# Kernel tuning notes

Hardware: AMD Instinct MI355X
Metric: run time of the kernel (lower is better)

## Reference

```python
import jax, jax.numpy as jnp
import numpy as np

B, T, E, H2, V, NT = 256, 192, 300, 256, 11626, 13  # batch, max_len, embed, hidden_dim, vocab, num_tags
START, STOP = 0, 10
NEG = -10000.0


def setup_inputs() -> dict:
    key = jax.random.key(0)
    ks = jax.random.split(key, 13)
    H = H2 // 2
    s = 0.1
    trans = jax.random.normal(ks[12], (NT, NT), dtype=jnp.float32)
    trans = trans.at[START, :].set(NEG).at[:, STOP].set(NEG)
    return {
        "sentence": jax.random.randint(ks[0], (B, T), 0, V),
        "seq_len": jax.random.randint(ks[1], (B,), 1, T + 1),  # lengths >= 1
        "tags": jax.random.randint(ks[2], (B, T), 0, 10),
        "embedding": jax.random.normal(ks[3], (V, E), dtype=jnp.float32) * s,
        "W_ih_f": jax.random.normal(ks[4], (4 * H, E), dtype=jnp.float32) * s,
        "W_hh_f": jax.random.normal(ks[5], (4 * H, H), dtype=jnp.float32) * s,
        "b_f": jnp.zeros((4 * H,), jnp.float32),
        "W_ih_b": jax.random.normal(ks[6], (4 * H, E), dtype=jnp.float32) * s,
        "W_hh_b": jax.random.normal(ks[7], (4 * H, H), dtype=jnp.float32) * s,
        "b_b": jnp.zeros((4 * H,), jnp.float32),
        "W_fc": jax.random.normal(ks[8], (NT, H2), dtype=jnp.float32) * s,
        "b_fc": jnp.zeros((NT,), jnp.float32),
        "transitions": trans,
    }


def _rev_within_len(x, lens):
    # reverse each sequence's first `len` positions (mimics packed-sequence reverse dir)
    t = jnp.arange(x.shape[1])
    idx = jnp.where(t[None, :] < lens[:, None], lens[:, None] - 1 - t[None, :], t[None, :])
    return jnp.take_along_axis(x, idx[:, :, None], axis=1)


def _lstm_dir(x, lens, W_ih, W_hh, b):
    # x: [B,T,E] -> [B,T,H]; PyTorch gate order i,f,g,o; padded steps frozen + zeroed output
    Bx, Tx, _ = x.shape
    H = W_hh.shape[1]
    mask = (jnp.arange(Tx)[None, :] < lens[:, None]).astype(x.dtype)  # [B,T]
    gx = jnp.einsum('bte,ge->btg', x, W_ih) + b  # precompute input projections

    def step(carry, inp):
        h, c = carry
        g_x, m = inp  # [B,4H], [B,1]
        g = g_x + h @ W_hh.T
        i, f, gg, o = jnp.split(g, 4, axis=-1)
        c_new = jax.nn.sigmoid(f) * c + jax.nn.sigmoid(i) * jnp.tanh(gg)
        h_new = jax.nn.sigmoid(o) * jnp.tanh(c_new)
        h = jnp.where(m > 0, h_new, h)
        c = jnp.where(m > 0, c_new, c)
        return (h, c), h * m

    h0 = jnp.zeros((Bx, H), x.dtype)
    _, hs = jax.lax.scan(step, (h0, h0), (gx.transpose(1, 0, 2), mask.T[:, :, None]))
    return hs.transpose(1, 0, 2)


def _crf_nll(feats, tags, transitions):
    # feats: [B,T,NT]; iterate over ALL T padded positions (faithful to source)
    def fwd_step(alpha, feat):
        # alpha_new[b,j] = logsumexp_i(alpha[b,i] + trans[j,i]) + feat[b,j]
        nxt = jax.nn.logsumexp(alpha[:, None, :] + transitions[None, :, :], axis=-1) + feat
        return nxt, None

    alpha0 = jnp.full((feats.shape[0], NT), NEG, feats.dtype).at[:, START].set(0.0)
    alphaT, _ = jax.lax.scan(fwd_step, alpha0, feats.transpose(1, 0, 2))
    fwd_score = jax.nn.logsumexp(alphaT + transitions[STOP][None, :], axis=-1)  # [B]

    tags_ext = jnp.concatenate([jnp.full((feats.shape[0], 1), START, tags.dtype), tags], axis=1)
    trans_sc = transitions[tags_ext[:, 1:], tags_ext[:, :-1]].sum(-1)
    emit_sc = jnp.take_along_axis(feats, tags[:, :, None], axis=2)[:, :, 0].sum(-1)
    gold = trans_sc + emit_sc + transitions[STOP, tags[:, -1]]
    return fwd_score - gold  # [B]


def reference(sentence, seq_len, tags, embedding, W_ih_f, W_hh_f, b_f,
              W_ih_b, W_hh_b, b_b, W_fc, b_fc, transitions):
    lens = jnp.clip(seq_len, 1, T)  # seq_len.clamp(max=192)
    emb = embedding[sentence]  # [B,T,E]
    h_f = _lstm_dir(emb, lens, W_ih_f, W_hh_f, b_f)
    h_b = _rev_within_len(_lstm_dir(_rev_within_len(emb, lens), lens, W_ih_b, W_hh_b, b_b), lens)
    out = jnp.concatenate([h_f, h_b], axis=-1)  # [B,T,H2]
    feats = jnp.einsum('bth,gh->btg', out, W_fc) + b_fc  # [B,T,NT]
    nll = _crf_nll(feats, tags, transitions)
    return nll.mean()
```

## Files before the change

kernel.cpp:

```cpp
#include <hip/hip_runtime.h>
#include <hip/hip_bf16.h>


#define B_   256
#define T_   192
#define E_   300
#define KP   320
#define H_   128
#define G4   512
#define NG   1024
#define NT_  13
#define NEGV -10000.0f
#define HSTR 144

typedef __attribute__((ext_vector_type(8))) short bf16x8;
typedef __attribute__((ext_vector_type(4))) float f32x4;
typedef __attribute__((ext_vector_type(4))) unsigned short u16x4;

__device__ __forceinline__ unsigned short f2bf(float f) {
    return (unsigned short)(__float_as_uint(f) >> 16);
}
__device__ __forceinline__ float bf2f(unsigned short h) {
    return __uint_as_float(((unsigned)h) << 16);
}
__device__ __forceinline__ float sigf(float x) {
    return __builtin_amdgcn_rcpf(1.0f + __expf(-x));
}
__device__ __forceinline__ float tanhfast(float x) {
    return __builtin_amdgcn_rcpf(1.0f + __expf(-2.0f * x)) * 2.0f - 1.0f;
}
__device__ __forceinline__ void barrier_lgkm() {
    asm volatile("s_waitcnt lgkmcnt(0)\n\ts_barrier" ::: "memory");
}

__global__ void pack_kernel(const float* __restrict__ Wf, const float* __restrict__ Wb,
                            const float* __restrict__ Whf, const float* __restrict__ Whb,
                            const float* __restrict__ emb, const int* __restrict__ sent,
                            unsigned short* __restrict__ Wp, unsigned short* __restrict__ Whp,
                            unsigned short* __restrict__ A) {
    int blk = blockIdx.x;
    int k = threadIdx.x;
    if (blk < NG) {
        float v = 0.0f;
        if (k < E_) v = (blk < G4) ? Wf[blk * E_ + k] : Wb[(blk - G4) * E_ + k];
        Wp[blk * KP + k] = f2bf(v);
    } else if (blk < NG + 1024) {
        int t = blk - NG;
        int d = t >> 9, g = t & 511;
        if (k < H_) {
            const float* src = d ? Whb : Whf;
            float v = src[g * H_ + k];
            int w = (g >> 4) & 7, j = g >> 7, colq = g & 15;
            int kc = k >> 5, quad = (k >> 3) & 3, e = k & 7;
            Whp[((((size_t)(d * 8 + w) * 4 + j) * 4 + kc) * 64 + quad * 16 + colq) * 8 + e] = f2bf(v);
        }
    } else {
        int m = blk - NG - 1024;
        int tok = sent[m];
        float v = 0.0f;
        if (k < E_) v = emb[(size_t)tok * E_ + k];
        A[(size_t)m * KP + k] = f2bf(v);
    }
}

__global__ __launch_bounds__(256, 2) void gemm_kernel(const unsigned short* __restrict__ A,
                                                      const unsigned short* __restrict__ Bw,
                                                      const float* __restrict__ bF,
                                                      const float* __restrict__ bB,
                                                      unsigned short* __restrict__ C) {
    __shared__ __align__(16) unsigned short As[128 * 64];
    __shared__ __align__(16) unsigned short Bs[128 * 64];
    const int tid  = threadIdx.x;
    const int lane = tid & 63;
    const int wave = tid >> 6;
    const int wr = wave >> 1, wc = wave & 1;
    const int colL = lane & 15;
    const int mBase = blockIdx.y * 128;
    const int bx = blockIdx.x;
    const int d  = bx >> 2;
    const int w0 = (bx & 3) * 2;
    f32x4 acc[4][4] = {};
    for (int k0 = 0; k0 < KP; k0 += 64) {
        #pragma unroll
        for (int j = 0; j < 4; j++) {
            int c   = tid + 256 * j;
            int row = c >> 3;
            int col = (c & 7) * 8;
            *(uint4*)(As + row * 64 + col) = *(const uint4*)(A + (size_t)(mBase + row) * KP + k0 + col);
            int ws = row >> 6, jj = (row >> 4) & 3, cc = row & 15;
            int srcrow = d * 512 + (8 * jj + w0 + ws) * 16 + cc;
            *(uint4*)(Bs + row * 64 + col) = *(const uint4*)(Bw + (size_t)srcrow * KP + k0 + col);
        }
        __syncthreads();
        #pragma unroll
        for (int ks = 0; ks < 2; ks++) {
            bf16x8 af[4], bfr[4];
            #pragma unroll
            for (int i = 0; i < 4; i++) {
                int arow = wr * 64 + i * 16 + colL;
                af[i]  = *(const bf16x8*)(As + arow * 64 + ks * 32 + (lane >> 4) * 8);
                int brow = wc * 64 + i * 16 + colL;
                bfr[i] = *(const bf16x8*)(Bs + brow * 64 + ks * 32 + (lane >> 4) * 8);
            }
            #pragma unroll
            for (int i = 0; i < 4; i++)
                #pragma unroll
                for (int n2 = 0; n2 < 4; n2++)
                    acc[i][n2] = __builtin_amdgcn_mfma_f32_16x16x32_bf16(af[i], bfr[n2], acc[i][n2], 0, 0, 0);
        }
        __syncthreads();
    }
    const float* bias_d = d ? bB : bF;
    float bj[4];
    #pragma unroll
    for (int n2 = 0; n2 < 4; n2++) bj[n2] = bias_d[(8 * n2 + w0 + wc) * 16 + colL];
    #pragma unroll
    for (int i = 0; i < 4; i++)
        #pragma unroll
        for (int r = 0; r < 4; r++) {
            int row = mBase + wr * 64 + i * 16 + (lane >> 4) * 4 + r;
            u16x4 v;
            #pragma unroll
            for (int n2 = 0; n2 < 4; n2++) v[n2] = f2bf(acc[i][n2][r] + bj[n2]);
            *(u16x4*)(C + (size_t)row * NG + d * 512 + (w0 + wc) * 64 + colL * 4) = v;
        }
}

__global__ __launch_bounds__(576, 1) void lstm_kernel(const unsigned short* __restrict__ gxP,
                                                      const unsigned short* __restrict__ Whp,
                                                      const int* __restrict__ seq_len,
                                                      const float* __restrict__ Wfc,
                                                      float* __restrict__ featsF,
                                                      float* __restrict__ featsB) {
    __shared__ __align__(16) unsigned short hL[2][16 * HSTR];
    __shared__ int Ls[4];
    __shared__ int maxLs;
    const int tid  = threadIdx.x;
    const int wave = tid >> 6;
    const int lane = tid & 63;
    const int col  = lane & 15;
    const int quad = lane >> 4;
    const int dir  = blockIdx.x & 1;
    const int b0   = (blockIdx.x >> 1) * 4;
    float* fOut = dir ? featsB : featsF;

    if (tid < 4) Ls[tid] = min(max(seq_len[b0 + tid], 1), T_);
    __syncthreads();
    if (tid == 0) { int m = 0; for (int i = 0; i < 4; i++) m = max(m, Ls[i]); maxLs = m; }
    __syncthreads();
    const int maxL = maxLs;
    const int Lq = Ls[quad];
    const int dNG = dir ? -NG : NG;

    bf16x8 Bf[4][4];
    bf16x8 Wf8[4];
    const unsigned short* rb = nullptr;
    int ofs2 = 0;
    u16x4 gx0v = {}, gx1v = {};
    float* fb = nullptr;
    int foff = 0;

    if (wave < 8) {
        #pragma unroll
        for (int j = 0; j < 4; j++)
            #pragma unroll
            for (int kc = 0; kc < 4; kc++)
                Bf[j][kc] = *(const bf16x8*)(Whp +
                    ((((size_t)(dir * 8 + wave) * 4 + j) * 4 + kc) * 64 + lane) * 8);
        int row = b0 + quad;
        int p0 = dir ? (Lq - 1) : 0;
        rb = gxP + ((size_t)(row * T_ + p0)) * NG + dir * 512 + wave * 64 + col * 4;
        gx0v = *(const u16x4*)(rb);
        gx1v = *(const u16x4*)(rb + ((Lq > 1) ? dNG : 0));
        ofs2 = min(2, Lq - 1) * dNG;
    } else {
        #pragma unroll
        for (int kc = 0; kc < 4; kc++)
            #pragma unroll
            for (int e = 0; e < 8; e++) {
                float v = (col < NT_) ? Wfc[col * 256 + dir * H_ + kc * 32 + quad * 8 + e] : 0.0f;
                Wf8[kc][e] = (short)f2bf(v);
            }
        fb = fOut + (size_t)(b0 + quad) * T_ * NT_ + col;
        foff = (dir ? (Lq - 1) : 0) * NT_;
    }
    const int fd = dir ? -NT_ : NT_;

    float cst = 0.0f;
    bf16x8 Af[4];
    #pragma unroll
    for (int kc = 0; kc < 4; kc++)
        #pragma unroll
        for (int e = 0; e < 8; e++) Af[kc][e] = 0;

    auto step_body = [&](int s, u16x4& gxs, int par) {
        if (wave < 8) {
            f32x4 acc[4];
            #pragma unroll
            for (int j = 0; j < 4; j++) {
                acc[j][0] = bf2f(gxs[j]);
                acc[j][1] = 0.f; acc[j][2] = 0.f; acc[j][3] = 0.f;
            }
            gxs = *(const u16x4*)(rb + ofs2);
            ofs2 = (s + 3 < Lq) ? ofs2 + dNG : ofs2;
            #pragma unroll
            for (int kc = 0; kc < 4; kc++)
                #pragma unroll
                for (int j = 0; j < 4; j++)
                    acc[j] = __builtin_amdgcn_mfma_f32_16x16x32_bf16(Af[kc], Bf[j][kc], acc[j], 0, 0, 0);
            float cn = sigf(acc[1][0]) * cst + sigf(acc[0][0]) * tanhfast(acc[2][0]);
            cst = cn;
            float hn = sigf(acc[3][0]) * tanhfast(cn);
            hL[par][(quad * 4) * HSTR + wave * 16 + col] = f2bf(hn);
        }
        barrier_lgkm();
        #pragma unroll
        for (int kc = 0; kc < 4; kc++)
            Af[kc] = *(const bf16x8*)(&hL[par][col * HSTR + kc * 32 + quad * 8]);
        if (wave == 8) {
            f32x4 fc = (f32x4){0.f, 0.f, 0.f, 0.f};
            #pragma unroll
            for (int kc = 0; kc < 4; kc++)
                fc = __builtin_amdgcn_mfma_f32_16x16x32_bf16(Af[kc], Wf8[kc], fc, 0, 0, 0);
            if (col < NT_ && s < Lq) fb[foff] = fc[0];
            foff += fd;
        }
    };

    for (int s = 0; s < maxL; s += 2) {
        step_body(s, gx0v, 0);
        if (s + 1 < maxL) step_body(s + 1, gx1v, 1);
    }
}

__global__ __launch_bounds__(64) void crf_kernel(const float* __restrict__ fF,
                                                 const float* __restrict__ fB,
                                                 const float* __restrict__ bfc,
                                                 const float* __restrict__ trans,
                                                 const int* __restrict__ tags,
                                                 const int* __restrict__ seq_len,
                                                 float* __restrict__ nll) {
    __shared__ __align__(16) float al[16];
    __shared__ __align__(16) float feat_lds[2 * 208];
    __shared__ float Tlds[NT_ * NT_];
    const int lane = threadIdx.x;
    const int b = blockIdx.x;
    const int Lb = min(max(seq_len[b], 1), T_);
    const float* fFb = fF + (size_t)b * T_ * NT_;
    const float* fBb = fB + (size_t)b * T_ * NT_;
    const int* tg = tags + (size_t)b * T_;

    for (int i = lane; i < NT_ * NT_; i += 64) Tlds[i] = trans[i];

    const int jc = min(lane, NT_ - 1);
    float Tj[NT_];
    #pragma unroll
    for (int i = 0; i < NT_; i++) Tj[i] = trans[jc * NT_ + i];
    const float bj  = bfc[jc];
    const float T10 = trans[10 * NT_ + jc];
    if (lane < NT_) al[lane] = (lane == 0) ? 0.0f : NEGV;

    const int e0 = lane * 4;
    const bool ldact = (lane < 52);
    float4 vF = {}, vB = {};
    if (ldact) { vF = *(const float4*)(fFb + e0); vB = *(const float4*)(fBb + e0); }

    #pragma unroll 1
    for (int c = 0; c < 12; ++c) {
        if (ldact) {
            float4 w;
            #pragma unroll
            for (int k = 0; k < 4; k++) {
                unsigned g = (unsigned)(c * 208 + e0 + k);
                unsigned t = g / 13u;
                float s = ((const float*)&vF)[k] + ((const float*)&vB)[k];
                ((float*)&w)[k] = (t < (unsigned)Lb) ? s : 0.0f;
            }
            *(float4*)&feat_lds[(c & 1) * 208 + e0] = w;
            if (c < 11) {
                vF = *(const float4*)(fFb + (c + 1) * 208 + e0);
                vB = *(const float4*)(fBb + (c + 1) * 208 + e0);
            }
        }
        barrier_lgkm();
        const int fbase = (c & 1) * 208;
        for (int tt = 0; tt < 16; ++tt) {
            float4 A0 = *(const float4*)&al[0];
            float4 A1 = *(const float4*)&al[4];
            float4 A2 = *(const float4*)&al[8];
            float a12 = al[12];
            float feat = feat_lds[fbase + tt * NT_ + jc];
            float v0 = A0.x + Tj[0],  v1 = A0.y + Tj[1],  v2 = A0.z + Tj[2],  v3 = A0.w + Tj[3];
            float v4 = A1.x + Tj[4],  v5 = A1.y + Tj[5],  v6 = A1.z + Tj[6],  v7 = A1.w + Tj[7];
            float v8 = A2.x + Tj[8],  v9 = A2.y + Tj[9],  v10 = A2.z + Tj[10], v11 = A2.w + Tj[11];
            float v12 = a12 + Tj[12];
            float p0 = fmaxf(v0, v1), p1 = fmaxf(v2, v3), p2 = fmaxf(v4, v5);
            float p3 = fmaxf(v6, v7), p4 = fmaxf(v8, v9), p5 = fmaxf(v10, v11);
            float q0 = fmaxf(p0, p1), q1 = fmaxf(p2, p3), q2 = fmaxf(p4, p5);
            float m = fmaxf(fmaxf(q0, q1), fmaxf(q2, v12));
            float e0_ = __expf(v0 - m),  e1_ = __expf(v1 - m),  e2_ = __expf(v2 - m);
            float e3_ = __expf(v3 - m),  e4_ = __expf(v4 - m),  e5_ = __expf(v5 - m);
            float e6_ = __expf(v6 - m),  e7_ = __expf(v7 - m),  e8_ = __expf(v8 - m);
            float e9_ = __expf(v9 - m),  e10_ = __expf(v10 - m), e11_ = __expf(v11 - m);
            float e12_ = __expf(v12 - m);
            float s0 = e0_ + e1_, s1 = e2_ + e3_, s2 = e4_ + e5_, s3 = e6_ + e7_;
            float s4 = e8_ + e9_, s5 = e10_ + e11_;
            float u0 = s0 + s1, u1 = s2 + s3, u2 = s4 + s5;
            float ss = (u0 + u1) + (u2 + e12_);
            float alnew = m + __logf(ss) + feat + bj;
            barrier_lgkm();
            if (lane < NT_) al[lane] = alnew;
            barrier_lgkm();
        }
    }

    float gp = 0.0f;
    #pragma unroll
    for (int u = 0; u < 3; ++u) {
        int t = lane + u * 64;
        int tt_ = tg[t];
        int pv = (t == 0) ? 0 : tg[t - 1];
        float e = bfc[tt_];
        if (t < Lb) e += fFb[t * NT_ + tt_] + fBb[t * NT_ + tt_];
        gp += Tlds[tt_ * NT_ + pv] + e;
    }
    #pragma unroll
    for (int o = 32; o > 0; o >>= 1) gp += __shfl_down(gp, o, 64);

    float vj = (lane < NT_) ? (al[lane] + T10) : -3.0e38f;
    float mm = vj;
    #pragma unroll
    for (int o = 32; o > 0; o >>= 1) mm = fmaxf(mm, __shfl_down(mm, o, 64));
    mm = __shfl(mm, 0, 64);
    float se = (lane < NT_) ? __expf(vj - mm) : 0.0f;
    #pragma unroll
    for (int o = 32; o > 0; o >>= 1) se += __shfl_down(se, o, 64);
    if (lane == 0) {
        float fwd = mm + __logf(se);
        float gold = gp + Tlds[10 * NT_ + tg[T_ - 1]];
        nll[b] = fwd - gold;
    }
}

__global__ void reduce_mean_kernel(const float* __restrict__ nll, float* __restrict__ out) {
    int tid = threadIdx.x;
    float v = nll[tid];
    for (int o = 32; o > 0; o >>= 1) v += __shfl_down(v, o, 64);
    __shared__ float wsum[4];
    if ((tid & 63) == 0) wsum[tid >> 6] = v;
    __syncthreads();
    if (tid == 0) out[0] = (wsum[0] + wsum[1] + wsum[2] + wsum[3]) * (1.0f / 256.0f);
}

extern "C" void kernel_launch(void* const* d_in, const int* in_sizes, int n_in,
                              void* d_out, int out_size, void* d_ws, size_t ws_size,
                              hipStream_t stream) {
    const int*   sentence  = (const int*)d_in[0];
    const int*   seq_len   = (const int*)d_in[1];
    const int*   tags      = (const int*)d_in[2];
    const float* embedding = (const float*)d_in[3];
    const float* W_ih_f    = (const float*)d_in[4];
    const float* W_hh_f    = (const float*)d_in[5];
    const float* b_f       = (const float*)d_in[6];
    const float* W_ih_b    = (const float*)d_in[7];
    const float* W_hh_b    = (const float*)d_in[8];
    const float* b_b       = (const float*)d_in[9];
    const float* W_fc      = (const float*)d_in[10];
    const float* b_fc      = (const float*)d_in[11];
    const float* trans     = (const float*)d_in[12];
    float* out = (float*)d_out;

    char* ws = (char*)d_ws;
    const size_t M = (size_t)B_ * T_;
    unsigned short* Wp    = (unsigned short*)(ws);
    unsigned short* Ap    = (unsigned short*)(ws + 655360);
    unsigned short* gx    = (unsigned short*)(ws + 32112640);
    float* featsF = (float*)(ws + 132775936);
    float* featsB = (float*)(ws + 135331840);
    float* nll    = (float*)(ws + 137887744);
    unsigned short* Whp   = (unsigned short*)(ws + 137888768);

    pack_kernel<<<NG + 1024 + (int)M, KP, 0, stream>>>(W_ih_f, W_ih_b, W_hh_f, W_hh_b,
                                                       embedding, sentence, Wp, Whp, Ap);
    dim3 gg(8, (int)(M / 128));
    gemm_kernel<<<gg, 256, 0, stream>>>(Ap, Wp, b_f, b_b, gx);
    lstm_kernel<<<128, 576, 0, stream>>>(gx, Whp, seq_len, W_fc, featsF, featsB);
    crf_kernel<<<B_, 64, 0, stream>>>(featsF, featsB, b_fc, trans, tags, seq_len, nll);
    reduce_mean_kernel<<<1, 256, 0, stream>>>(nll, out);
}
```

Before: 330.2 us.

## Split LSTM recurrent MFMA chains, use direct global-to-LDS loads, fuse mean reduction

The LSTM step now splits the four-deep dependent MFMA accumulation chain into two independent two-deep chains per gate and adds the input projection afterwards. This shortens the serial latency on the recurrent critical path. The GEMM tile loads now use global_load_lds to write straight into shared memory instead of staging through registers, and occupancy is raised to 3 blocks per CU. The final mean kernel is removed in favour of a per-block atomicAdd plus a memset, which makes the float summation order nondeterministic.

Result: slower. 349.3 us (+5.8%).

```diff
diff --git a/kernel.cpp b/kernel.cpp
--- a/kernel.cpp
+++ b/kernel.cpp
@@ -63,7 +63,7 @@
     }
 }
 
-__global__ __launch_bounds__(256, 2) void gemm_kernel(const unsigned short* __restrict__ A,
+__global__ __launch_bounds__(256, 3) void gemm_kernel(const unsigned short* __restrict__ A,
                                                       const unsigned short* __restrict__ Bw,
                                                       const float* __restrict__ bF,
                                                       const float* __restrict__ bB,
@@ -86,10 +86,14 @@
             int c   = tid + 256 * j;
             int row = c >> 3;
             int col = (c & 7) * 8;
-            *(uint4*)(As + row * 64 + col) = *(const uint4*)(A + (size_t)(mBase + row) * KP + k0 + col);
+            __builtin_amdgcn_global_load_lds(
+                (const void*)(A + (size_t)(mBase + row) * KP + k0 + col),
+                (void*)((char*)As + c * 16), 16, 0, 0);
             int ws = row >> 6, jj = (row >> 4) & 3, cc = row & 15;
             int srcrow = d * 512 + (8 * jj + w0 + ws) * 16 + cc;
-            *(uint4*)(Bs + row * 64 + col) = *(const uint4*)(Bw + (size_t)srcrow * KP + k0 + col);
+            __builtin_amdgcn_global_load_lds(
+                (const void*)(Bw + (size_t)srcrow * KP + k0 + col),
+                (void*)((char*)Bs + c * 16), 16, 0, 0);
         }
         __syncthreads();
         #pragma unroll
@@ -187,6 +191,7 @@
     const int fd = dir ? -NT_ : NT_;
 
     float cst = 0.0f;
+    const f32x4 zc = (f32x4){0.f, 0.f, 0.f, 0.f};
     bf16x8 Af[4];
     #pragma unroll
     for (int kc = 0; kc < 4; kc++)
@@ -195,22 +200,27 @@
 
     auto step_body = [&](int s, u16x4& gxs, int par) {
         if (wave < 8) {
-            f32x4 acc[4];
-            #pragma unroll
-            for (int j = 0; j < 4; j++) {
-                acc[j][0] = bf2f(gxs[j]);
-                acc[j][1] = 0.f; acc[j][2] = 0.f; acc[j][3] = 0.f;
-            }
+            u16x4 cur = gxs;
             gxs = *(const u16x4*)(rb + ofs2);
             ofs2 = (s + 3 < Lq) ? ofs2 + dNG : ofs2;
-            #pragma unroll
-            for (int kc = 0; kc < 4; kc++)
-                #pragma unroll
-                for (int j = 0; j < 4; j++)
-                    acc[j] = __builtin_amdgcn_mfma_f32_16x16x32_bf16(Af[kc], Bf[j][kc], acc[j], 0, 0, 0);
-            float cn = sigf(acc[1][0]) * cst + sigf(acc[0][0]) * tanhfast(acc[2][0]);
+            f32x4 pa[4], pb[4];
+            #pragma unroll
+            for (int j = 0; j < 4; j++) {
+                pa[j] = __builtin_amdgcn_mfma_f32_16x16x32_bf16(Af[0], Bf[j][0], zc, 0, 0, 0);
+                pb[j] = __builtin_amdgcn_mfma_f32_16x16x32_bf16(Af[1], Bf[j][1], zc, 0, 0, 0);
+            }
+            #pragma unroll
+            for (int j = 0; j < 4; j++) {
+                pa[j] = __builtin_amdgcn_mfma_f32_16x16x32_bf16(Af[2], Bf[j][2], pa[j], 0, 0, 0);
+                pb[j] = __builtin_amdgcn_mfma_f32_16x16x32_bf16(Af[3], Bf[j][3], pb[j], 0, 0, 0);
+            }
+            float g0 = pa[0][0] + pb[0][0] + bf2f(cur[0]);
+            float g1 = pa[1][0] + pb[1][0] + bf2f(cur[1]);
+            float g2 = pa[2][0] + pb[2][0] + bf2f(cur[2]);
+            float g3 = pa[3][0] + pb[3][0] + bf2f(cur[3]);
+            float cn = sigf(g1) * cst + sigf(g0) * tanhfast(g2);
             cst = cn;
-            float hn = sigf(acc[3][0]) * tanhfast(cn);
+            float hn = sigf(g3) * tanhfast(cn);
             hL[par][(quad * 4) * HSTR + wave * 16 + col] = f2bf(hn);
         }
         barrier_lgkm();
@@ -239,7 +249,7 @@
                                                  const float* __restrict__ trans,
                                                  const int* __restrict__ tags,
                                                  const int* __restrict__ seq_len,
-                                                 float* __restrict__ nll) {
+                                                 float* __restrict__ out) {
     __shared__ __align__(16) float al[16];
     __shared__ __align__(16) float feat_lds[2 * 208];
     __shared__ float Tlds[NT_ * NT_];
@@ -338,18 +348,8 @@
     if (lane == 0) {
         float fwd = mm + __logf(se);
         float gold = gp + Tlds[10 * NT_ + tg[T_ - 1]];
-        nll[b] = fwd - gold;
-    }
-}
-
-__global__ void reduce_mean_kernel(const float* __restrict__ nll, float* __restrict__ out) {
-    int tid = threadIdx.x;
-    float v = nll[tid];
-    for (int o = 32; o > 0; o >>= 1) v += __shfl_down(v, o, 64);
-    __shared__ float wsum[4];
-    if ((tid & 63) == 0) wsum[tid >> 6] = v;
-    __syncthreads();
-    if (tid == 0) out[0] = (wsum[0] + wsum[1] + wsum[2] + wsum[3]) * (1.0f / 256.0f);
+        atomicAdd(out, (fwd - gold) * (1.0f / 256.0f));
+    }
 }
 
 extern "C" void kernel_launch(void* const* d_in, const int* in_sizes, int n_in,
@@ -377,14 +377,13 @@
     unsigned short* gx    = (unsigned short*)(ws + 32112640);
     float* featsF = (float*)(ws + 132775936);
     float* featsB = (float*)(ws + 135331840);
-    float* nll    = (float*)(ws + 137887744);
-    unsigned short* Whp   = (unsigned short*)(ws + 137888768);
-
+    unsigned short* Whp   = (unsigned short*)(ws + 137887744);
+
+    hipMemsetAsync(out, 0, sizeof(float), stream);
     pack_kernel<<<NG + 1024 + (int)M, KP, 0, stream>>>(W_ih_f, W_ih_b, W_hh_f, W_hh_b,
                                                        embedding, sentence, Wp, Whp, Ap);
     dim3 gg(8, (int)(M / 128));
     gemm_kernel<<<gg, 256, 0, stream>>>(Ap, Wp, b_f, b_b, gx);
     lstm_kernel<<<128, 576, 0, stream>>>(gx, Whp, seq_len, W_fc, featsF, featsB);
-    crf_kernel<<<B_, 64, 0, stream>>>(featsF, featsB, b_fc, trans, tags, seq_len, nll);
-    reduce_mean_kernel<<<1, 256, 0, stream>>>(nll, out);
-}
+    crf_kernel<<<B_, 64, 0, stream>>>(featsF, featsB, b_fc, trans, tags, seq_len, out);
+}
```
